# Optimization experiments

Hardware: AMD Instinct MI355X
Metric: run time of the kernel (lower is better)

The kernel has to match this reference:

```python
import jax, jax.numpy as jnp
import numpy as np

B, S, T = 4096, 32, 32   # batch (flattened words), source chars, target chars
V = 256                  # char vocab (source and target)
E, H, A = 128, 64, 64    # source embed, GRU units, attention dim
BOW = 1                  # begin-of-word token id


def setup_inputs() -> dict:
    key = jax.random.key(0)
    ks = iter(jax.random.split(key, 32))
    p = lambda shape: jax.random.normal(next(ks), shape, dtype=jnp.float32) * 0.05
    return {
        "src_ids": jax.random.randint(next(ks), (B, S), 0, V, dtype=jnp.int64),
        "tgt_ids": jax.random.randint(next(ks), (B, T), 0, V, dtype=jnp.int64),
        "src_emb": p((V, E)),
        "enc_Wf": p((E, 3 * H)), "enc_Uf": p((H, 3 * H)), "enc_bf": p((2, 3 * H)),
        "enc_Wb": p((E, 3 * H)), "enc_Ub": p((H, 3 * H)), "enc_bb": p((2, 3 * H)),
        "attn_We": p((H, A)), "attn_be": p((A,)),
        "attn_Wd": p((H, A)), "attn_bd": p((A,)),
        "attn_v": p((A, 1)), "attn_bv": p((1,)),
        "dec_W": p((H + H, 3 * H)), "dec_U": p((H, 3 * H)), "dec_b": p((2, 3 * H)),
        "out_W": p((H, V)), "out_b": p((V,)),
    }


def _gru_cell(h, x, W, U, b):
    # TF GRUCell with reset_after=True (default): separate input/recurrent biases
    xp = x @ W + b[0]
    hp = h @ U + b[1]
    xz, xr, xh = jnp.split(xp, 3, axis=-1)
    hz, hr, hh = jnp.split(hp, 3, axis=-1)
    z = jax.nn.sigmoid(xz + hz)
    r = jax.nn.sigmoid(xr + hr)
    n = jnp.tanh(xh + r * hh)
    return z * h + (1.0 - z) * n


def _gru_scan(xs, h0, W, U, b):
    # xs: [S, B, D] -> outputs [S, B, H]
    def step(h, x):
        h_new = _gru_cell(h, x, W, U, b)
        return h_new, h_new
    _, ys = jax.lax.scan(step, h0, xs)
    return ys


def reference(src_ids, tgt_ids, src_emb,
              enc_Wf, enc_Uf, enc_bf, enc_Wb, enc_Ub, enc_bb,
              attn_We, attn_be, attn_Wd, attn_bd, attn_v, attn_bv,
              dec_W, dec_U, dec_b, out_W, out_b):
    batch = src_ids.shape[0]
    # --- encoder: embedding + bidirectional GRU (merge_mode='sum') ---
    emb = src_emb[src_ids]                       # [B,S,E]
    xs = jnp.swapaxes(emb, 0, 1)                 # [S,B,E]
    h0 = jnp.zeros((batch, H), emb.dtype)
    fwd = _gru_scan(xs, h0, enc_Wf, enc_Uf, enc_bf)
    bwd = _gru_scan(xs[::-1], h0, enc_Wb, enc_Ub, enc_bb)[::-1]
    encoded = jnp.swapaxes(fwd + bwd, 0, 1)      # [B,S,H]

    # --- attention memory setup ---
    enc_proj = encoded @ attn_We + attn_be       # [B,S,A]

    # --- decoder inputs: BOW-prefixed teacher-forced targets, tied embedding ---
    dec_in = jnp.concatenate(
        [jnp.full((batch, 1), BOW, dtype=tgt_ids.dtype), tgt_ids[:, :-1]], axis=1)
    tied_table = out_W.T * jnp.sqrt(jnp.asarray(H, encoded.dtype))  # [V,H]
    dec_emb = tied_table[dec_in]                 # [B,T,H]

    # --- decoder: Bahdanau-attention GRU, scan over time ---
    def step(h, x):
        dproj = h @ attn_Wd + attn_bd                        # [B,A]
        s = jnp.tanh(dproj[:, None, :] + enc_proj)           # [B,S,A]
        logit = (s @ attn_v)[..., 0] + attn_bv[0]            # [B,S]
        w = jax.nn.softmax(logit, axis=1)                    # softmax over S
        ctx = jnp.einsum('bs,bsh->bh', w, encoded)           # [B,H]
        att_in = jnp.concatenate([x, ctx], axis=1)           # [B,2H]
        h_new = _gru_cell(h, att_in, dec_W, dec_U, dec_b)
        return h_new, h_new

    _, hs = jax.lax.scan(step, encoded[:, 0], jnp.swapaxes(dec_emb, 0, 1))
    hidden = jnp.swapaxes(hs, 0, 1)              # [B,T,H]
    logits = hidden @ out_W + out_b              # [B,T,V]
    return logits
```

## Files before the change

### kernel.cpp

```cpp
#include <hip/hip_runtime.h>
#include <hip/hip_bf16.h>

typedef unsigned short u16;
typedef __bf16  bf16x8 __attribute__((ext_vector_type(8)));
typedef float   f32x4  __attribute__((ext_vector_type(4)));
typedef unsigned int   u32x4 __attribute__((ext_vector_type(4)));
typedef unsigned short u16x4 __attribute__((ext_vector_type(4)));

union FragU { bf16x8 v; u16 u[8]; u32x4 q; };

__device__ __forceinline__ float b2f(u16 u) {
    unsigned int x = ((unsigned int)u) << 16;
    return __builtin_bit_cast(float, x);
}
__device__ __forceinline__ u16 f2b(float f) {
    unsigned int x = __builtin_bit_cast(unsigned int, f);
    unsigned int r = (x + 0x7fffu + ((x >> 16) & 1u)) >> 16;
    return (u16)r;
}
__device__ __forceinline__ float rcp_(float x) { return __builtin_amdgcn_rcpf(x); }
__device__ __forceinline__ float sigm_(float x) { return rcp_(1.0f + __expf(-x)); }
__device__ __forceinline__ float tanh_(float x) {
    float e = __expf(2.0f * x);
    return 1.0f - 2.0f * rcp_(e + 1.0f);
}
__device__ __forceinline__ bf16x8 load_afrag(const u16* s) {
    FragU f; f.q = *(const u32x4*)s; return f.v;
}
__device__ __forceinline__ f32x4 mfma16(bf16x8 a, bf16x8 b, f32x4 c) {
    return __builtin_amdgcn_mfma_f32_16x16x32_bf16(a, b, c, 0, 0, 0);
}
__device__ __forceinline__ void split2(float f, u16& hi, u16& lo) {
    hi = f2b(f); lo = f2b(f - b2f(hi));
}

template<int MODE, int K, int N>
__global__ __launch_bounds__(256, (MODE >= 2) ? 2 : 1) void gemm_hl(
    const float* __restrict__ srcf, const u16* __restrict__ sh,
    const u16* __restrict__ sl, const u16* __restrict__ sh2,
    const u16* __restrict__ sl2, const float* __restrict__ W,
    const float* __restrict__ bias, float* __restrict__ outf,
    u16* __restrict__ outh)
{
    constexpr int KP = K + 8;
    constexpr int LK = (K == 128) ? 7 : 6;
    __shared__ __attribute__((aligned(16))) u16 Ash[64 * KP];
    __shared__ __attribute__((aligned(16))) u16 Asl[64 * KP];

    const int tid  = threadIdx.x;
    const int lane = tid & 63, w = tid >> 6;
    const int q = lane >> 4, ln = lane & 15;
    const int rbase = blockIdx.x * 64;

    for (int i = tid; i < 64 * K; i += 256) {
        int r = i >> LK, c = i & (K - 1);
        int rg = rbase + r;
        float f;
        if constexpr (MODE == 0)      f = srcf[rg * K + c];
        else if constexpr (MODE == 1) f = srcf[c * 256 + rg] * 8.0f;
        else if constexpr (MODE == 2)
            f = b2f(sh[rg * 64 + c]) + b2f(sl[rg * 64 + c])
              + b2f(sh2[rg * 64 + c]) + b2f(sl2[rg * 64 + c]);
        else                          f = b2f(sh[rg * 64 + c]) + b2f(sl[rg * 64 + c]);
        u16 hi, lo; split2(f, hi, lo);
        Ash[r * KP + c] = hi; Asl[r * KP + c] = lo;
    }

    constexpr int NT  = N / 64;
    constexpr int NKF = K / 32;
    FragU bfh[NT][NKF], bfl[NT][NKF];
    float bv[NT];
    const int cw = w * (N >> 2);
#pragma unroll
    for (int tl = 0; tl < NT; ++tl) {
        int col = cw + tl * 16 + ln;
#pragma unroll
        for (int kf = 0; kf < NKF; ++kf)
#pragma unroll
            for (int j = 0; j < 8; ++j) {
                float f = W[(kf * 32 + q * 8 + j) * N + col];
                split2(f, bfh[tl][kf].u[j], bfl[tl][kf].u[j]);
            }
        bv[tl] = bias[col];
    }
    __syncthreads();

#pragma unroll
    for (int r = 0; r < 4; ++r) {
        bf16x8 afh[NKF], afl[NKF];
#pragma unroll
        for (int kf = 0; kf < NKF; ++kf) {
            afh[kf] = load_afrag(&Ash[(r * 16 + ln) * KP + kf * 32 + q * 8]);
            afl[kf] = load_afrag(&Asl[(r * 16 + ln) * KP + kf * 32 + q * 8]);
        }
#pragma unroll
        for (int tl = 0; tl < NT; ++tl) {
            f32x4 acc = {0.f, 0.f, 0.f, 0.f};
#pragma unroll
            for (int kf = 0; kf < NKF; ++kf) {
                acc = mfma16(afl[kf], bfh[tl][kf].v, acc);
                acc = mfma16(afh[kf], bfl[tl][kf].v, acc);
                acc = mfma16(afh[kf], bfh[tl][kf].v, acc);
            }
            const int col = cw + tl * 16 + ln;
#pragma unroll
            for (int i = 0; i < 4; ++i) {
                int rowg = rbase + r * 16 + q * 4 + i;
                float val = acc[i] + bv[tl];
                if constexpr (MODE == 2) {
                    int b = rowg >> 5, s2 = rowg & 31;
                    outh[(b * 64 + col) * 32 + s2] = f2b(val * 2.0f);
                } else if constexpr (MODE == 3) {
                    outf[rowg * N + col] = val;
                } else {
                    outf[rowg * 192 + col] = val;
                }
            }
        }
    }
}

__global__ __launch_bounds__(256, 2) void enc8(
    const int* __restrict__ src_ids, const float* __restrict__ xf,
    const float* __restrict__ xb,
    const float* __restrict__ Uf_, const float* __restrict__ bf_,
    const float* __restrict__ Ub_, const float* __restrict__ bb_,
    u16* __restrict__ fh, u16* __restrict__ fl,
    u16* __restrict__ bh, u16* __restrict__ bl)
{
    __shared__ __attribute__((aligned(16))) u16 hsh[16 * 72];
    __shared__ __attribute__((aligned(16))) u16 hsl[16 * 72];
    const int tid  = threadIdx.x;
    const int lane = tid & 63, w = tid >> 6;
    const int q = lane >> 4, ln = lane & 15;
    const int dir = (int)(blockIdx.x >> 9);
    const int b0  = (int)(blockIdx.x & 511) * 8;
    const float* xpv = dir ? xb  : xf;
    const float* U   = dir ? Ub_ : Uf_;
    const float* b_  = dir ? bb_ : bf_;
    u16* oh = dir ? bh : fh;
    u16* ol = dir ? bl : fl;
    const int jw = w * 16;
    const bool rowok = (q < 2);

    for (int i = tid; i < 16 * 64; i += 256) {
        int r = i >> 6, c = i & 63;
        hsh[r * 72 + c] = 0; hsl[r * 72 + c] = 0;
    }
    FragU ufh[3][2], ufl[3][2];
    float b1[3];
#pragma unroll
    for (int g = 0; g < 3; ++g) {
        int col = g * 64 + jw + ln;
#pragma unroll
        for (int kf = 0; kf < 2; ++kf)
#pragma unroll
            for (int j = 0; j < 8; ++j) {
                float f = U[(kf * 32 + q * 8 + j) * 192 + col];
                split2(f, ufh[g][kf].u[j], ufl[g][kf].u[j]);
            }
        b1[g] = b_[192 + col];
    }
    float hp[4] = {0, 0, 0, 0};

    float xg[3][4];
    {
        const int s0 = dir ? 31 : 0;
#pragma unroll
        for (int i = 0; i < 4; ++i) {
            int rowv = b0 + ((q * 4 + i) & 7);
            int id = src_ids[rowv * 32 + s0];
#pragma unroll
            for (int g = 0; g < 3; ++g) xg[g][i] = xpv[id * 192 + g * 64 + jw + ln];
        }
    }
    __syncthreads();

    for (int step = 0; step < 32; ++step) {
        const int s = dir ? (31 - step) : step;
        float xgn[3][4];
        {
            int sn = dir ? (step >= 31 ? 0 : 30 - step) : (step >= 31 ? 31 : step + 1);
#pragma unroll
            for (int i = 0; i < 4; ++i) {
                int rowv = b0 + ((q * 4 + i) & 7);
                int id = src_ids[rowv * 32 + sn];
#pragma unroll
                for (int g = 0; g < 3; ++g) xgn[g][i] = xpv[id * 192 + g * 64 + jw + ln];
            }
        }
        bf16x8 a0h = load_afrag(&hsh[ln * 72 + q * 8]);
        bf16x8 a1h = load_afrag(&hsh[ln * 72 + 32 + q * 8]);
        bf16x8 a0l = load_afrag(&hsl[ln * 72 + q * 8]);
        bf16x8 a1l = load_afrag(&hsl[ln * 72 + 32 + q * 8]);
        f32x4 acc[3];
#pragma unroll
        for (int g = 0; g < 3; ++g) {
            f32x4 a = {0.f, 0.f, 0.f, 0.f};
            a = mfma16(a0l, ufh[g][0].v, a);
            a = mfma16(a0h, ufl[g][0].v, a);
            a = mfma16(a0h, ufh[g][0].v, a);
            a = mfma16(a1l, ufh[g][1].v, a);
            a = mfma16(a1h, ufl[g][1].v, a);
            a = mfma16(a1h, ufh[g][1].v, a);
            acc[g] = a;
        }
        float nh[4];
#pragma unroll
        for (int i = 0; i < 4; ++i) {
            const int rowg = b0 + q * 4 + i;
            float zz = sigm_(xg[0][i] + acc[0][i] + b1[0]);
            float rr = sigm_(xg[1][i] + acc[1][i] + b1[1]);
            float nn = tanh_(xg[2][i] + rr * (acc[2][i] + b1[2]));
            nh[i] = zz * hp[i] + (1.0f - zz) * nn;  hp[i] = nh[i];
            if (rowok) {
                const int gidx = (rowg * 32 + s) * 64 + jw + ln;
                u16 hi, lo; split2(nh[i], hi, lo);
                oh[gidx] = hi; ol[gidx] = lo;
            }
        }
        __syncthreads();
        if (rowok) {
#pragma unroll
            for (int i = 0; i < 4; ++i) {
                u16 hi, lo; split2(nh[i], hi, lo);
                hsh[(q * 4 + i) * 72 + jw + ln] = hi;
                hsl[(q * 4 + i) * 72 + jw + ln] = lo;
            }
        }
        __syncthreads();
#pragma unroll
        for (int g = 0; g < 3; ++g)
#pragma unroll
            for (int i = 0; i < 4; ++i) xg[g][i] = xgn[g][i];
    }
}

__global__ __launch_bounds__(256, 1) void dec_kernel(
    const int* __restrict__ tgt_ids, const float* __restrict__ xpvd,
    const u16* __restrict__ fh, const u16* __restrict__ fl,
    const u16* __restrict__ bh, const u16* __restrict__ bl,
    const u16* __restrict__ encpT,
    const float* __restrict__ dec_U, const float* __restrict__ dec_W,
    const float* __restrict__ dec_b,
    const float* __restrict__ Wd, const float* __restrict__ bd,
    const float* __restrict__ v_, const float* __restrict__ bv_,
    u16* __restrict__ hid_hi, u16* __restrict__ hid_lo)
{
    __shared__ __attribute__((aligned(16))) float enc_lds[8 * 2048];
    __shared__ __attribute__((aligned(16))) u16 hqh[16 * 72];
    __shared__ __attribute__((aligned(16))) u16 hql[16 * 72];
    __shared__ __attribute__((aligned(16))) u16 cxh[16 * 72];
    __shared__ __attribute__((aligned(16))) u16 cxl[16 * 72];
    __shared__ __attribute__((aligned(16))) float edl[8 * 72];
    __shared__ float wl[8 * 36];
    __shared__ float vl[64];
    const int tid  = threadIdx.x;
    const int lane = tid & 63, w = tid >> 6;
    const int q = lane >> 4, ln = lane & 15;
    const int b0 = blockIdx.x * 8;
    const int jw = w * 16;
    const bool rowok = (q < 2);

    {
        const u16* g0 = fh + (size_t)b0 * 2048;
        const u16* g1 = fl + (size_t)b0 * 2048;
        const u16* g2 = bh + (size_t)b0 * 2048;
        const u16* g3 = bl + (size_t)b0 * 2048;
        for (int i = tid; i < 8 * 2048 / 4; i += 256) {
            u16x4 v0 = *(const u16x4*)(g0 + i * 4);
            u16x4 v1 = *(const u16x4*)(g1 + i * 4);
            u16x4 v2 = *(const u16x4*)(g2 + i * 4);
            u16x4 v3 = *(const u16x4*)(g3 + i * 4);
            f32x4 f;
#pragma unroll
            for (int k = 0; k < 4; ++k)
                f[k] = (b2f(v0[k]) + b2f(v1[k])) + (b2f(v2[k]) + b2f(v3[k]));
            *(f32x4*)(&enc_lds[i * 4]) = f;
        }
    }
    if (tid < 64) vl[tid] = v_[tid];
    const float bv0 = bv_[0];

    FragU wdh[2], wdl[2], ufh[3][2], ufl[3][2], wch[3][2], wcl[3][2];
    float b1[3];
#pragma unroll
    for (int kf = 0; kf < 2; ++kf)
#pragma unroll
        for (int j = 0; j < 8; ++j) {
            float f = Wd[(kf * 32 + q * 8 + j) * 64 + jw + ln];
            split2(f, wdh[kf].u[j], wdl[kf].u[j]);
        }
#pragma unroll
    for (int g = 0; g < 3; ++g) {
        int col = g * 64 + jw + ln;
#pragma unroll
        for (int kf = 0; kf < 2; ++kf)
#pragma unroll
            for (int j = 0; j < 8; ++j) {
                int k = kf * 32 + q * 8 + j;
                float fu = dec_U[k * 192 + col];
                split2(fu, ufh[g][kf].u[j], ufl[g][kf].u[j]);
                float fc = dec_W[(64 + k) * 192 + col];
                split2(fc, wch[g][kf].u[j], wcl[g][kf].u[j]);
            }
        b1[g] = dec_b[192 + col];
    }
    const float bd_ = bd[jw + ln];

    float Ee[64];
    {
        const int bb2 = tid >> 5, ss = tid & 31;
        const u16* ep = &encpT[(size_t)(b0 + bb2) * 2048 + ss];
#pragma unroll
        for (int a = 0; a < 64; ++a) Ee[a] = __expf(b2f(ep[a * 32]));
    }

    float xg[3][4];
#pragma unroll
    for (int g = 0; g < 3; ++g) {
        float f = xpvd[1 * 192 + g * 64 + jw + ln];
#pragma unroll
        for (int i = 0; i < 4; ++i) xg[g][i] = f;
    }
    __syncthreads();

    float SVB = bv0;
#pragma unroll
    for (int a = 0; a < 64; ++a) SVB += vl[a];

    for (int i = tid; i < 16 * 64; i += 256) {
        int r = i >> 6, c = i & 63;
        if (r < 8) {
            u16 hi, lo; split2(enc_lds[r * 2048 + c], hi, lo);
            hqh[r * 72 + c] = hi; hql[r * 72 + c] = lo;
        } else {
            hqh[r * 72 + c] = 0; hql[r * 72 + c] = 0;
            cxh[r * 72 + c] = 0; cxl[r * 72 + c] = 0;
        }
    }
    float hp[4];
#pragma unroll
    for (int i = 0; i < 4; ++i)
        hp[i] = rowok ? enc_lds[(q * 4 + i) * 2048 + jw + ln] : 0.f;
    __syncthreads();

    for (int t = 0; t < 32; ++t) {
        float xgn[3][4];
        {
            int tn = (t >= 31) ? 30 : t;
#pragma unroll
            for (int i = 0; i < 4; ++i) {
                int rowv = b0 + ((q * 4 + i) & 7);
                int id = tgt_ids[rowv * 32 + tn];
#pragma unroll
                for (int g = 0; g < 3; ++g) xgn[g][i] = xpvd[id * 192 + g * 64 + jw + ln];
            }
        }
        bf16x8 ah0 = load_afrag(&hqh[ln * 72 + q * 8]);
        bf16x8 ah1 = load_afrag(&hqh[ln * 72 + 32 + q * 8]);
        bf16x8 al0 = load_afrag(&hql[ln * 72 + q * 8]);
        bf16x8 al1 = load_afrag(&hql[ln * 72 + 32 + q * 8]);
        {
            f32x4 a = {0.f, 0.f, 0.f, 0.f};
            a = mfma16(al0, wdh[0].v, a);
            a = mfma16(ah0, wdl[0].v, a);
            a = mfma16(ah0, wdh[0].v, a);
            a = mfma16(al1, wdh[1].v, a);
            a = mfma16(ah1, wdl[1].v, a);
            a = mfma16(ah1, wdh[1].v, a);
            if (rowok) {
#pragma unroll
                for (int i = 0; i < 4; ++i)
                    edl[(q * 4 + i) * 72 + jw + ln] = __expf((a[i] + bd_) * 2.0f);
            }
        }
        __syncthreads();
        {
            const int bb2 = tid >> 5, sidx = tid & 31;
            const float* dp = &edl[bb2 * 72];
            float av0 = 0.f, av1 = 0.f, av2 = 0.f, av3 = 0.f;
#pragma unroll
            for (int a4 = 0; a4 < 16; ++a4) {
                f32x4 dv = *(const f32x4*)(dp + a4 * 4);
                av0 += vl[a4 * 4 + 0] * rcp_(__builtin_fmaf(dv[0], Ee[a4 * 4 + 0], 1.0f));
                av1 += vl[a4 * 4 + 1] * rcp_(__builtin_fmaf(dv[1], Ee[a4 * 4 + 1], 1.0f));
                av2 += vl[a4 * 4 + 2] * rcp_(__builtin_fmaf(dv[2], Ee[a4 * 4 + 2], 1.0f));
                av3 += vl[a4 * 4 + 3] * rcp_(__builtin_fmaf(dv[3], Ee[a4 * 4 + 3], 1.0f));
            }
            float logit = SVB - 2.0f * ((av0 + av1) + (av2 + av3));
            float m = logit;
#pragma unroll
            for (int off = 16; off > 0; off >>= 1) m = fmaxf(m, __shfl_xor(m, off, 32));
            float e2 = __expf(logit - m);
            float ssum = e2;
#pragma unroll
            for (int off = 16; off > 0; off >>= 1) ssum += __shfl_xor(ssum, off, 32);
            wl[bb2 * 36 + sidx] = e2 * rcp_(ssum);
        }
        __syncthreads();
#pragma unroll
        for (int rr2 = 0; rr2 < 2; ++rr2) {
            const int b = rr2 * 4 + w;
            float c0 = 0.f, c1 = 0.f, c2 = 0.f, c3 = 0.f;
#pragma unroll
            for (int s4 = 0; s4 < 8; ++s4) {
                const int s = s4 * 4 + q;
                const float ww = wl[b * 36 + s];
                f32x4 ev = *(const f32x4*)(&enc_lds[b * 2048 + s * 64 + ln * 4]);
                c0 += ww * ev[0]; c1 += ww * ev[1];
                c2 += ww * ev[2]; c3 += ww * ev[3];
            }
            c0 += __shfl_xor(c0, 16); c0 += __shfl_xor(c0, 32);
            c1 += __shfl_xor(c1, 16); c1 += __shfl_xor(c1, 32);
            c2 += __shfl_xor(c2, 16); c2 += __shfl_xor(c2, 32);
            c3 += __shfl_xor(c3, 16); c3 += __shfl_xor(c3, 32);
            if (q == 0) {
                u16x4 vh, vo;
                u16 th, tl2;
                split2(c0, th, tl2); vh[0] = th; vo[0] = tl2;
                split2(c1, th, tl2); vh[1] = th; vo[1] = tl2;
                split2(c2, th, tl2); vh[2] = th; vo[2] = tl2;
                split2(c3, th, tl2); vh[3] = th; vo[3] = tl2;
                *(u16x4*)(&cxh[b * 72 + ln * 4]) = vh;
                *(u16x4*)(&cxl[b * 72 + ln * 4]) = vo;
            }
        }
        __syncthreads();
        bf16x8 ac0 = load_afrag(&cxh[ln * 72 + q * 8]);
        bf16x8 ac1 = load_afrag(&cxh[ln * 72 + 32 + q * 8]);
        bf16x8 al2 = load_afrag(&cxl[ln * 72 + q * 8]);
        bf16x8 al3 = load_afrag(&cxl[ln * 72 + 32 + q * 8]);
        f32x4 ax[3], ahh[3];
#pragma unroll
        for (int g = 0; g < 3; ++g) {
            f32x4 a = {0.f, 0.f, 0.f, 0.f};
            a = mfma16(al2, wch[g][0].v, a);
            a = mfma16(ac0, wcl[g][0].v, a);
            a = mfma16(ac0, wch[g][0].v, a);
            a = mfma16(al3, wch[g][1].v, a);
            a = mfma16(ac1, wcl[g][1].v, a);
            a = mfma16(ac1, wch[g][1].v, a);
            ax[g] = a;
            f32x4 h = {0.f, 0.f, 0.f, 0.f};
            h = mfma16(al0, ufh[g][0].v, h);
            h = mfma16(ah0, ufl[g][0].v, h);
            h = mfma16(ah0, ufh[g][0].v, h);
            h = mfma16(al1, ufh[g][1].v, h);
            h = mfma16(ah1, ufl[g][1].v, h);
            h = mfma16(ah1, ufh[g][1].v, h);
            ahh[g] = h;
        }
        float nh[4];
#pragma unroll
        for (int i = 0; i < 4; ++i) {
            int rowg = b0 + q * 4 + i;
            float zz = sigm_(xg[0][i] + ax[0][i] + ahh[0][i] + b1[0]);
            float rr = sigm_(xg[1][i] + ax[1][i] + ahh[1][i] + b1[1]);
            float nn = tanh_(xg[2][i] + ax[2][i] + rr * (ahh[2][i] + b1[2]));
            nh[i] = zz * hp[i] + (1.0f - zz) * nn;  hp[i] = nh[i];
            if (rowok) {
                int gidx = (rowg * 32 + t) * 64 + jw + ln;
                u16 hi, lo; split2(nh[i], hi, lo);
                hid_hi[gidx] = hi; hid_lo[gidx] = lo;
                hqh[(q * 4 + i) * 72 + jw + ln] = hi;
                hql[(q * 4 + i) * 72 + jw + ln] = lo;
            }
        }
        __syncthreads();
#pragma unroll
        for (int g = 0; g < 3; ++g)
#pragma unroll
            for (int i = 0; i < 4; ++i) xg[g][i] = xgn[g][i];
    }
}

extern "C" void kernel_launch(void* const* d_in, const int* in_sizes, int n_in,
                              void* d_out, int out_size, void* d_ws, size_t ws_size,
                              hipStream_t stream) {
    const int*   src_ids = (const int*)d_in[0];
    const int*   tgt_ids = (const int*)d_in[1];
    const float* src_emb = (const float*)d_in[2];
    const float* enc_Wf  = (const float*)d_in[3];
    const float* enc_Uf  = (const float*)d_in[4];
    const float* enc_bf  = (const float*)d_in[5];
    const float* enc_Wb  = (const float*)d_in[6];
    const float* enc_Ub  = (const float*)d_in[7];
    const float* enc_bb  = (const float*)d_in[8];
    const float* attn_We = (const float*)d_in[9];
    const float* attn_be = (const float*)d_in[10];
    const float* attn_Wd = (const float*)d_in[11];
    const float* attn_bd = (const float*)d_in[12];
    const float* attn_v  = (const float*)d_in[13];
    const float* attn_bv = (const float*)d_in[14];
    const float* dec_W   = (const float*)d_in[15];
    const float* dec_U   = (const float*)d_in[16];
    const float* dec_b   = (const float*)d_in[17];
    const float* out_W   = (const float*)d_in[18];
    const float* out_b   = (const float*)d_in[19];

    u16* ws = (u16*)d_ws;
    u16* fwd_hi = ws;
    u16* fwd_lo = ws +  8388608;
    u16* bwd_hi = ws + 16777216;
    u16* bwd_lo = ws + 25165824;
    u16* encpT  = ws + 33554432;
    float* xpv_f = (float*)(ws + 41943040);
    float* xpv_b = (float*)(ws + 42041344);
    float* xpvd  = (float*)(ws + 42139648);
    u16* hid_hi = fwd_hi;
    u16* hid_lo = fwd_lo;

    dim3 blk(256);
    gemm_hl<0, 128, 192><<<4, blk, 0, stream>>>(
        src_emb, nullptr, nullptr, nullptr, nullptr, enc_Wf, enc_bf, xpv_f, nullptr);
    gemm_hl<0, 128, 192><<<4, blk, 0, stream>>>(
        src_emb, nullptr, nullptr, nullptr, nullptr, enc_Wb, enc_bb, xpv_b, nullptr);
    gemm_hl<1, 64, 192><<<4, blk, 0, stream>>>(
        out_W, nullptr, nullptr, nullptr, nullptr, dec_W, dec_b, xpvd, nullptr);
    enc8<<<1024, blk, 0, stream>>>(src_ids, xpv_f, xpv_b, enc_Uf, enc_bf,
                                   enc_Ub, enc_bb, fwd_hi, fwd_lo, bwd_hi, bwd_lo);
    gemm_hl<2, 64, 64><<<2048, blk, 0, stream>>>(
        nullptr, fwd_hi, fwd_lo, bwd_hi, bwd_lo, attn_We, attn_be, nullptr, encpT);
    dec_kernel<<<512, blk, 0, stream>>>(tgt_ids, xpvd, fwd_hi, fwd_lo, bwd_hi,
                                        bwd_lo, encpT, dec_U, dec_W, dec_b,
                                        attn_Wd, attn_bd, attn_v, attn_bv,
                                        hid_hi, hid_lo);
    gemm_hl<3, 64, 256><<<2048, blk, 0, stream>>>(
        nullptr, hid_hi, hid_lo, nullptr, nullptr, out_W, out_b, (float*)d_out, nullptr);
}
```

Baseline: 591.9 us.

## Pack two decoder row groups per 512-thread block and merge projection GEMMs

The three small input-projection GEMM launches become one kernel that dispatches on block index through a shared device body, removing two launches. The decoder now runs 512-thread blocks, each holding two independent 8-row batch groups with their own duplicated LDS buffers, giving 256 blocks instead of 512. This is meant to change how the latency-bound recurrent decoder fills CUs. In exchange, both halves share block-wide barriers, LDS use per block doubles, and the new launch bound caps registers per thread, which could cause spills given the large per-thread arrays.

New measurement: 985.0 us. 66.4% more time.

```diff
diff --git a/kernel.cpp b/kernel.cpp
--- a/kernel.cpp
+++ b/kernel.cpp
@@ -35,12 +35,12 @@
 }
 
 template<int MODE, int K, int N>
-__global__ __launch_bounds__(256, (MODE >= 2) ? 2 : 1) void gemm_hl(
+__device__ __forceinline__ void gemm_body(
     const float* __restrict__ srcf, const u16* __restrict__ sh,
     const u16* __restrict__ sl, const u16* __restrict__ sh2,
     const u16* __restrict__ sl2, const float* __restrict__ W,
     const float* __restrict__ bias, float* __restrict__ outf,
-    u16* __restrict__ outh)
+    u16* __restrict__ outh, int rbase)
 {
     constexpr int KP = K + 8;
     constexpr int LK = (K == 128) ? 7 : 6;
@@ -50,7 +50,6 @@
     const int tid  = threadIdx.x;
     const int lane = tid & 63, w = tid >> 6;
     const int q = lane >> 4, ln = lane & 15;
-    const int rbase = blockIdx.x * 64;
 
     for (int i = tid; i < 64 * K; i += 256) {
         int r = i >> LK, c = i & (K - 1);
@@ -118,6 +117,37 @@
             }
         }
     }
+}
+
+template<int MODE, int K, int N>
+__global__ __launch_bounds__(256, (MODE >= 2) ? 2 : 1) void gemm_hl(
+    const float* __restrict__ srcf, const u16* __restrict__ sh,
+    const u16* __restrict__ sl, const u16* __restrict__ sh2,
+    const u16* __restrict__ sl2, const float* __restrict__ W,
+    const float* __restrict__ bias, float* __restrict__ outf,
+    u16* __restrict__ outh)
+{
+    gemm_body<MODE, K, N>(srcf, sh, sl, sh2, sl2, W, bias, outf, outh,
+                          (int)blockIdx.x * 64);
+}
+
+__global__ __launch_bounds__(256, 1) void xpv_all(
+    const float* __restrict__ src_emb,
+    const float* __restrict__ Wf, const float* __restrict__ bf, float* __restrict__ xf,
+    const float* __restrict__ Wb, const float* __restrict__ bb, float* __restrict__ xb,
+    const float* __restrict__ outW, const float* __restrict__ dW,
+    const float* __restrict__ db, float* __restrict__ xd)
+{
+    const int b = blockIdx.x;
+    if (b < 4)
+        gemm_body<0, 128, 192>(src_emb, nullptr, nullptr, nullptr, nullptr,
+                               Wf, bf, xf, nullptr, b * 64);
+    else if (b < 8)
+        gemm_body<0, 128, 192>(src_emb, nullptr, nullptr, nullptr, nullptr,
+                               Wb, bb, xb, nullptr, (b - 4) * 64);
+    else
+        gemm_body<1, 64, 192>(outW, nullptr, nullptr, nullptr, nullptr,
+                              dW, db, xd, nullptr, (b - 8) * 64);
 }
 
 __global__ __launch_bounds__(256, 2) void enc8(
@@ -236,7 +266,7 @@
     }
 }
 
-__global__ __launch_bounds__(256, 1) void dec_kernel(
+__global__ __launch_bounds__(512, 2) void dec_kernel(
     const int* __restrict__ tgt_ids, const float* __restrict__ xpvd,
     const u16* __restrict__ fh, const u16* __restrict__ fl,
     const u16* __restrict__ bh, const u16* __restrict__ bl,
@@ -247,27 +277,34 @@
     const float* __restrict__ v_, const float* __restrict__ bv_,
     u16* __restrict__ hid_hi, u16* __restrict__ hid_lo)
 {
-    __shared__ __attribute__((aligned(16))) float enc_lds[8 * 2048];
-    __shared__ __attribute__((aligned(16))) u16 hqh[16 * 72];
-    __shared__ __attribute__((aligned(16))) u16 hql[16 * 72];
-    __shared__ __attribute__((aligned(16))) u16 cxh[16 * 72];
-    __shared__ __attribute__((aligned(16))) u16 cxl[16 * 72];
-    __shared__ __attribute__((aligned(16))) float edl[8 * 72];
-    __shared__ float wl[8 * 36];
+    __shared__ __attribute__((aligned(16))) float enc_lds[2][8 * 2048];
+    __shared__ __attribute__((aligned(16))) u16 hqh[2][16 * 72];
+    __shared__ __attribute__((aligned(16))) u16 hql[2][16 * 72];
+    __shared__ __attribute__((aligned(16))) u16 cxh[2][16 * 72];
+    __shared__ __attribute__((aligned(16))) u16 cxl[2][16 * 72];
+    __shared__ __attribute__((aligned(16))) float edl[2][8 * 72];
+    __shared__ float wl[2][8 * 36];
     __shared__ float vl[64];
     const int tid  = threadIdx.x;
-    const int lane = tid & 63, w = tid >> 6;
+    const int t2   = tid & 255;
+    const int half = tid >> 8;
+    const int lane = t2 & 63, w = t2 >> 6;
     const int q = lane >> 4, ln = lane & 15;
-    const int b0 = blockIdx.x * 8;
+    const int b0 = blockIdx.x * 16 + half * 8;
     const int jw = w * 16;
     const bool rowok = (q < 2);
+
+    float* encL = enc_lds[half];
+    u16*  hqhL = hqh[half];  u16* hqlL = hql[half];
+    u16*  cxhL = cxh[half];  u16* cxlL = cxl[half];
+    float* edlL = edl[half]; float* wlL = wl[half];
 
     {
         const u16* g0 = fh + (size_t)b0 * 2048;
         const u16* g1 = fl + (size_t)b0 * 2048;
         const u16* g2 = bh + (size_t)b0 * 2048;
         const u16* g3 = bl + (size_t)b0 * 2048;
-        for (int i = tid; i < 8 * 2048 / 4; i += 256) {
+        for (int i = t2; i < 8 * 2048 / 4; i += 256) {
             u16x4 v0 = *(const u16x4*)(g0 + i * 4);
             u16x4 v1 = *(const u16x4*)(g1 + i * 4);
             u16x4 v2 = *(const u16x4*)(g2 + i * 4);
@@ -276,7 +313,7 @@
 #pragma unroll
             for (int k = 0; k < 4; ++k)
                 f[k] = (b2f(v0[k]) + b2f(v1[k])) + (b2f(v2[k]) + b2f(v3[k]));
-            *(f32x4*)(&enc_lds[i * 4]) = f;
+            *(f32x4*)(&encL[i * 4]) = f;
         }
     }
     if (tid < 64) vl[tid] = v_[tid];
@@ -310,7 +347,7 @@
 
     float Ee[64];
     {
-        const int bb2 = tid >> 5, ss = tid & 31;
+        const int bb2 = t2 >> 5, ss = t2 & 31;
         const u16* ep = &encpT[(size_t)(b0 + bb2) * 2048 + ss];
 #pragma unroll
         for (int a = 0; a < 64; ++a) Ee[a] = __expf(b2f(ep[a * 32]));
@@ -329,20 +366,20 @@
 #pragma unroll
     for (int a = 0; a < 64; ++a) SVB += vl[a];
 
-    for (int i = tid; i < 16 * 64; i += 256) {
+    for (int i = t2; i < 16 * 64; i += 256) {
         int r = i >> 6, c = i & 63;
         if (r < 8) {
-            u16 hi, lo; split2(enc_lds[r * 2048 + c], hi, lo);
-            hqh[r * 72 + c] = hi; hql[r * 72 + c] = lo;
+            u16 hi, lo; split2(encL[r * 2048 + c], hi, lo);
+            hqhL[r * 72 + c] = hi; hqlL[r * 72 + c] = lo;
         } else {
-            hqh[r * 72 + c] = 0; hql[r * 72 + c] = 0;
-            cxh[r * 72 + c] = 0; cxl[r * 72 + c] = 0;
+            hqhL[r * 72 + c] = 0; hqlL[r * 72 + c] = 0;
+            cxhL[r * 72 + c] = 0; cxlL[r * 72 + c] = 0;
         }
     }
     float hp[4];
 #pragma unroll
     for (int i = 0; i < 4; ++i)
-        hp[i] = rowok ? enc_lds[(q * 4 + i) * 2048 + jw + ln] : 0.f;
+        hp[i] = rowok ? encL[(q * 4 + i) * 2048 + jw + ln] : 0.f;
     __syncthreads();
 
     for (int t = 0; t < 32; ++t) {
@@ -357,10 +394,10 @@
                 for (int g = 0; g < 3; ++g) xgn[g][i] = xpvd[id * 192 + g * 64 + jw + ln];
             }
         }
-        bf16x8 ah0 = load_afrag(&hqh[ln * 72 + q * 8]);
-        bf16x8 ah1 = load_afrag(&hqh[ln * 72 + 32 + q * 8]);
-        bf16x8 al0 = load_afrag(&hql[ln * 72 + q * 8]);
-        bf16x8 al1 = load_afrag(&hql[ln * 72 + 32 + q * 8]);
+        bf16x8 ah0 = load_afrag(&hqhL[ln * 72 + q * 8]);
+        bf16x8 ah1 = load_afrag(&hqhL[ln * 72 + 32 + q * 8]);
+        bf16x8 al0 = load_afrag(&hqlL[ln * 72 + q * 8]);
+        bf16x8 al1 = load_afrag(&hqlL[ln * 72 + 32 + q * 8]);
         {
             f32x4 a = {0.f, 0.f, 0.f, 0.f};
             a = mfma16(al0, wdh[0].v, a);
@@ -372,13 +409,13 @@
             if (rowok) {
 #pragma unroll
                 for (int i = 0; i < 4; ++i)
-                    edl[(q * 4 + i) * 72 + jw + ln] = __expf((a[i] + bd_) * 2.0f);
+                    edlL[(q * 4 + i) * 72 + jw + ln] = __expf((a[i] + bd_) * 2.0f);
             }
         }
         __syncthreads();
         {
-            const int bb2 = tid >> 5, sidx = tid & 31;
-            const float* dp = &edl[bb2 * 72];
+            const int bb2 = t2 >> 5, sidx = t2 & 31;
+            const float* dp = &edlL[bb2 * 72];
             float av0 = 0.f, av1 = 0.f, av2 = 0.f, av3 = 0.f;
 #pragma unroll
             for (int a4 = 0; a4 < 16; ++a4) {
@@ -396,7 +433,7 @@
             float ssum = e2;
 #pragma unroll
             for (int off = 16; off > 0; off >>= 1) ssum += __shfl_xor(ssum, off, 32);
-            wl[bb2 * 36 + sidx] = e2 * rcp_(ssum);
+            wlL[bb2 * 36 + sidx] = e2 * rcp_(ssum);
         }
         __syncthreads();
 #pragma unroll
@@ -406,8 +443,8 @@
 #pragma unroll
             for (int s4 = 0; s4 < 8; ++s4) {
                 const int s = s4 * 4 + q;
-                const float ww = wl[b * 36 + s];
-                f32x4 ev = *(const f32x4*)(&enc_lds[b * 2048 + s * 64 + ln * 4]);
+                const float ww = wlL[b * 36 + s];
+                f32x4 ev = *(const f32x4*)(&encL[b * 2048 + s * 64 + ln * 4]);
                 c0 += ww * ev[0]; c1 += ww * ev[1];
                 c2 += ww * ev[2]; c3 += ww * ev[3];
             }
@@ -422,15 +459,15 @@
                 split2(c1, th, tl2); vh[1] = th; vo[1] = tl2;
                 split2(c2, th, tl2); vh[2] = th; vo[2] = tl2;
                 split2(c3, th, tl2); vh[3] = th; vo[3] = tl2;
-                *(u16x4*)(&cxh[b * 72 + ln * 4]) = vh;
-                *(u16x4*)(&cxl[b * 72 + ln * 4]) = vo;
+                *(u16x4*)(&cxhL[b * 72 + ln * 4]) = vh;
+                *(u16x4*)(&cxlL[b * 72 + ln * 4]) = vo;
             }
         }
         __syncthreads();
-        bf16x8 ac0 = load_afrag(&cxh[ln * 72 + q * 8]);
-        bf16x8 ac1 = load_afrag(&cxh[ln * 72 + 32 + q * 8]);
-        bf16x8 al2 = load_afrag(&cxl[ln * 72 + q * 8]);
-        bf16x8 al3 = load_afrag(&cxl[ln * 72 + 32 + q * 8]);
+        bf16x8 ac0 = load_afrag(&cxhL[ln * 72 + q * 8]);
+        bf16x8 ac1 = load_afrag(&cxhL[ln * 72 + 32 + q * 8]);
+        bf16x8 al2 = load_afrag(&cxlL[ln * 72 + q * 8]);
+        bf16x8 al3 = load_afrag(&cxlL[ln * 72 + 32 + q * 8]);
         f32x4 ax[3], ahh[3];
 #pragma unroll
         for (int g = 0; g < 3; ++g) {
@@ -463,8 +500,8 @@
                 int gidx = (rowg * 32 + t) * 64 + jw + ln;
                 u16 hi, lo; split2(nh[i], hi, lo);
                 hid_hi[gidx] = hi; hid_lo[gidx] = lo;
-                hqh[(q * 4 + i) * 72 + jw + ln] = hi;
-                hql[(q * 4 + i) * 72 + jw + ln] = lo;
+                hqhL[(q * 4 + i) * 72 + jw + ln] = hi;
+                hqlL[(q * 4 + i) * 72 + jw + ln] = lo;
             }
         }
         __syncthreads();
@@ -512,20 +549,18 @@
     u16* hid_lo = fwd_lo;
 
     dim3 blk(256);
-    gemm_hl<0, 128, 192><<<4, blk, 0, stream>>>(
-        src_emb, nullptr, nullptr, nullptr, nullptr, enc_Wf, enc_bf, xpv_f, nullptr);
-    gemm_hl<0, 128, 192><<<4, blk, 0, stream>>>(
-        src_emb, nullptr, nullptr, nullptr, nullptr, enc_Wb, enc_bb, xpv_b, nullptr);
-    gemm_hl<1, 64, 192><<<4, blk, 0, stream>>>(
-        out_W, nullptr, nullptr, nullptr, nullptr, dec_W, dec_b, xpvd, nullptr);
+    xpv_all<<<12, blk, 0, stream>>>(src_emb, enc_Wf, enc_bf, xpv_f,
+                                    enc_Wb, enc_bb, xpv_b,
+                                    out_W, dec_W, dec_b, xpvd);
     enc8<<<1024, blk, 0, stream>>>(src_ids, xpv_f, xpv_b, enc_Uf, enc_bf,
                                    enc_Ub, enc_bb, fwd_hi, fwd_lo, bwd_hi, bwd_lo);
     gemm_hl<2, 64, 64><<<2048, blk, 0, stream>>>(
         nullptr, fwd_hi, fwd_lo, bwd_hi, bwd_lo, attn_We, attn_be, nullptr, encpT);
-    dec_kernel<<<512, blk, 0, stream>>>(tgt_ids, xpvd, fwd_hi, fwd_lo, bwd_hi,
-                                        bwd_lo, encpT, dec_U, dec_W, dec_b,
-                                        attn_Wd, attn_bd, attn_v, attn_bv,
-                                        hid_hi, hid_lo);
+    dec_kernel<<<256, dim3(512), 0, stream>>>(tgt_ids, xpvd, fwd_hi, fwd_lo,
+                                              bwd_hi, bwd_lo, encpT,
+                                              dec_U, dec_W, dec_b,
+                                              attn_Wd, attn_bd, attn_v, attn_bv,
+                                              hid_hi, hid_lo);
     gemm_hl<3, 64, 256><<<2048, blk, 0, stream>>>(
         nullptr, hid_hi, hid_lo, nullptr, nullptr, out_W, out_b, (float*)d_out, nullptr);
 }
```
